# Kernel tuning notes

Hardware: AMD Instinct MI355X
Metric: run time of the kernel (lower is better)

Reference implementation:

```python
import math
import jax, jax.numpy as jnp
import numpy as np

B, T, D, S = 4, 8192, 1024, 32  # batch, seq, dim, num_slots; segment L = T // S


def setup_inputs() -> dict:
    key = jax.random.key(0)
    ks = jax.random.split(key, 11)
    d_inv_sqrt = D ** -0.5
    return {
        "x": jax.random.normal(ks[0], (B, T, D), jnp.float32),
        "gate_w": jax.random.normal(ks[1], (D, D), jnp.float32) * d_inv_sqrt,
        "gate_b": jnp.zeros((D,), jnp.float32),
        "read_q_w": jax.random.normal(ks[2], (D, D), jnp.float32) * 0.02,
        "read_k_w": jax.random.normal(ks[3], (D, D), jnp.float32) * 0.02,
        "read_v_w": jax.random.normal(ks[4], (D, D), jnp.float32) * 0.02,
        "output_w": jax.random.normal(ks[5], (D, D), jnp.float32) * d_inv_sqrt,
        "memory_slots": jax.random.normal(ks[6], (S, D), jnp.float32) * 0.02,
        "write_q_w": jax.random.normal(ks[7], (D, D), jnp.float32) * 0.02,
        "write_k_w": jax.random.normal(ks[8], (D, D), jnp.float32) * 0.02,
        "write_v_w": jax.random.normal(ks[9], (D, D), jnp.float32) * 0.02,
    }


def reference(x, gate_w, gate_b, read_q_w, read_k_w, read_v_w, output_w,
              memory_slots, write_q_w, write_k_w, write_v_w):
    b, t, d = x.shape
    s = memory_slots.shape[0]
    L = t // s  # segment length
    scale = 1.0 / math.sqrt(d)

    h = x @ gate_w.T + gate_b  # [B,T,D] gate pre-activation

    # --- write: per-slot attention over that slot's segment (block-diagonal) ---
    q = memory_slots @ write_q_w.T                      # [S,D]
    xs = x.reshape(b, s, L, d)                          # [B,S,L,D]
    k = xs @ write_k_w.T                                # [B,S,L,D]
    v = xs @ write_v_w.T                                # [B,S,L,D]
    wqk = jnp.einsum('sd,bsld->bsl', q, k) * scale      # [B,S,L]
    wattn = jax.nn.softmax(wqk, axis=-1)
    memory = jnp.einsum('bsl,bsld->bsd', wattn, v)      # [B,S,D]

    # --- read: masked cross-attention from tokens to memory slots ---
    rq = x @ read_q_w.T                                 # [B,T,D]
    rk = memory @ read_k_w.T                            # [B,S,D]
    rv = memory @ read_v_w.T                            # [B,S,D]
    rqk = jnp.einsum('btd,bsd->bts', rq, rk) * scale    # [B,T,S]
    seg = jnp.arange(t) // L                            # token -> segment index
    mask = seg[:, None] <= jnp.arange(s)[None, :]       # [T,S]; attend to slots >= own segment
    rqk = jnp.where(mask[None, :, :], rqk, -jnp.inf)
    rattn = jax.nn.softmax(rqk, axis=-1)
    read = jnp.einsum('bts,bsd->btd', rattn, rv)        # [B,T,D]

    y = x + jax.nn.sigmoid(h) * read
    out = y @ output_w.T
    return out, memory
```

## Files before the change

### kernel.cpp

```cpp
#include <hip/hip_runtime.h>
#include <stdint.h>

#define TB 4
#define TT 8192
#define TD 1024
#define TS 32
#define TL 256
#define BT 32768

typedef unsigned short u16;
typedef __bf16 bf16x8 __attribute__((ext_vector_type(8)));
typedef float f32x4 __attribute__((ext_vector_type(4)));

typedef uint32_t u32_g __attribute__((address_space(1)));
typedef uint32_t u32_l __attribute__((address_space(3)));

#define VMWAIT(N) asm volatile("s_waitcnt vmcnt(" #N ")" ::: "memory")
#define LGKM0()   asm volatile("s_waitcnt lgkmcnt(0)" ::: "memory")

__device__ __forceinline__ u16 f2b(float f){
  union { float f; uint32_t u; } a; a.f = f;
  uint32_t r = a.u + 0x7FFFu + ((a.u >> 16) & 1u);
  return (u16)(r >> 16);
}
__device__ __forceinline__ float b2f(u16 u){
  union { uint32_t u; float f; } a; a.u = ((uint32_t)u) << 16;
  return a.f;
}
__device__ __forceinline__ void gll16(const void* g, void* l){
  __builtin_amdgcn_global_load_lds((const u32_g*)g, (u32_l*)l, 16, 0, 0);
}
__device__ __forceinline__ bf16x8 cvt8(const float* p){
  float4 a = *(const float4*)p, b = *(const float4*)(p+4);
  union { u16 s[8]; bf16x8 v; } u;
  u.s[0]=f2b(a.x); u.s[1]=f2b(a.y); u.s[2]=f2b(a.z); u.s[3]=f2b(a.w);
  u.s[4]=f2b(b.x); u.s[5]=f2b(b.y); u.s[6]=f2b(b.z); u.s[7]=f2b(b.w);
  return u.v;
}

__global__ void k_convdot(const float* __restrict__ x, const float* __restrict__ qk,
                          u16* __restrict__ xb, float* __restrict__ wqk,
                          const float* __restrict__ s0, const float* __restrict__ s1,
                          const float* __restrict__ s2, const float* __restrict__ s3,
                          const float* __restrict__ s4,
                          u16* __restrict__ d0, u16* __restrict__ d1,
                          u16* __restrict__ d2, u16* __restrict__ d3,
                          u16* __restrict__ d4){
  int tid = threadIdx.x;
  if (blockIdx.x >= 2048){
    int i = (blockIdx.x - 2048)*256 + tid;
    int mi = i >> 18, j = i & 262143;
    const float* src; u16* dst;
    if      (mi == 0){ src = s0; dst = d0; }
    else if (mi == 1){ src = s1; dst = d1; }
    else if (mi == 2){ src = s2; dst = d2; }
    else if (mi == 3){ src = s3; dst = d3; }
    else             { src = s4; dst = d4; }
    float4 v = ((const float4*)src)[j];
    ushort4 u; u.x=f2b(v.x); u.y=f2b(v.y); u.z=f2b(v.z); u.w=f2b(v.w);
    ((ushort4*)dst)[j] = u;
    return;
  }
  int lane = tid & 63, wv = tid >> 6;
  long bt0 = (long)blockIdx.x * 16;
  int sseg = (int)((bt0 & (TT-1)) >> 8);
  float qv[16];
  #pragma unroll
  for (int i=0;i<4;i++){
    float4 t = *(const float4*)(qk + (size_t)sseg*TD + i*256 + lane*4);
    qv[i*4+0]=t.x; qv[i*4+1]=t.y; qv[i*4+2]=t.z; qv[i*4+3]=t.w;
  }
  for (int tok = wv; tok < 16; tok += 4){
    long bt = bt0 + tok;
    const float* xr = x + bt*TD;
    float dot = 0.f;
    #pragma unroll
    for (int i=0;i<4;i++){
      float4 t = *(const float4*)(xr + i*256 + lane*4);
      ushort4 u; u.x=f2b(t.x); u.y=f2b(t.y); u.z=f2b(t.z); u.w=f2b(t.w);
      *(ushort4*)(xb + bt*TD + i*256 + lane*4) = u;
      dot += t.x*qv[i*4] + t.y*qv[i*4+1] + t.z*qv[i*4+2] + t.w*qv[i*4+3];
    }
    #pragma unroll
    for (int o=32;o;o>>=1) dot += __shfl_xor(dot, o);
    if (lane == 0) wqk[bt] = dot;
  }
}

__global__ __launch_bounds__(512) void k_q32f(const float* __restrict__ ms, const float* __restrict__ Wq,
                                              float* __restrict__ q){
  int tid = threadIdx.x, lane = tid & 63, wv = tid >> 6;
  int r15 = lane & 15, kg = lane >> 4;
  int n0 = blockIdx.x*128 + wv*16;
  const float* ap = ms + (size_t)r15*TD + kg*8;
  const float* bp = Wq + (size_t)(n0 + r15)*TD + kg*8;
  f32x4 a0 = {0,0,0,0}, a1 = {0,0,0,0};
  #pragma unroll 4
  for (int k0=0; k0<TD; k0+=32){
    bf16x8 b  = cvt8(bp + k0);
    bf16x8 x0 = cvt8(ap + k0);
    bf16x8 x1 = cvt8(ap + 16*TD + k0);
    a0 = __builtin_amdgcn_mfma_f32_16x16x32_bf16(x0, b, a0, 0,0,0);
    a1 = __builtin_amdgcn_mfma_f32_16x16x32_bf16(x1, b, a1, 0,0,0);
  }
  #pragma unroll
  for (int qq=0; qq<4; ++qq){
    q[(size_t)(kg*4 + qq)*TD + n0 + r15]      = a0[qq];
    q[(size_t)(16 + kg*4 + qq)*TD + n0 + r15] = a1[qq];
  }
}

__global__ __launch_bounds__(512) void k_smm128(const u16* __restrict__ A,
                                                const u16* __restrict__ W0, const u16* __restrict__ W1,
                                                float* __restrict__ oF0, u16* __restrict__ oB0,
                                                u16* __restrict__ oBT1){
  int tid = threadIdx.x, lane = tid & 63, wv = tid >> 6;
  int r15 = lane & 15, kg = lane >> 4;
  int wr = wv >> 2, wc = wv & 3;
  int n0 = blockIdx.x*128 + wc*32;
  const u16* W = blockIdx.z ? W1 : W0;
  const u16* ap = A + (size_t)(wr*64 + r15)*TD + kg*8;
  const u16* bp = W + (size_t)(n0 + r15)*TD + kg*8;
  f32x4 acc[4][2];
  #pragma unroll
  for (int i=0;i<4;i++){ f32x4 z={0,0,0,0}; acc[i][0]=z; acc[i][1]=z; }
  #pragma unroll 2
  for (int k0=0; k0<TD; k0+=32){
    bf16x8 b0 = *(const bf16x8*)(bp + k0);
    bf16x8 b1 = *(const bf16x8*)(bp + 16*TD + k0);
    bf16x8 a0 = *(const bf16x8*)(ap + k0);
    bf16x8 a1 = *(const bf16x8*)(ap + 16*TD + k0);
    bf16x8 a2 = *(const bf16x8*)(ap + 32*TD + k0);
    bf16x8 a3 = *(const bf16x8*)(ap + 48*TD + k0);
    acc[0][0] = __builtin_amdgcn_mfma_f32_16x16x32_bf16(a0, b0, acc[0][0], 0,0,0);
    acc[0][1] = __builtin_amdgcn_mfma_f32_16x16x32_bf16(a0, b1, acc[0][1], 0,0,0);
    acc[1][0] = __builtin_amdgcn_mfma_f32_16x16x32_bf16(a1, b0, acc[1][0], 0,0,0);
    acc[1][1] = __builtin_amdgcn_mfma_f32_16x16x32_bf16(a1, b1, acc[1][1], 0,0,0);
    acc[2][0] = __builtin_amdgcn_mfma_f32_16x16x32_bf16(a2, b0, acc[2][0], 0,0,0);
    acc[2][1] = __builtin_amdgcn_mfma_f32_16x16x32_bf16(a2, b1, acc[2][1], 0,0,0);
    acc[3][0] = __builtin_amdgcn_mfma_f32_16x16x32_bf16(a3, b0, acc[3][0], 0,0,0);
    acc[3][1] = __builtin_amdgcn_mfma_f32_16x16x32_bf16(a3, b1, acc[3][1], 0,0,0);
  }
  #pragma unroll
  for (int mf=0; mf<4; ++mf){
    #pragma unroll
    for (int nf=0; nf<2; ++nf){
      int n = n0 + nf*16 + r15;
      #pragma unroll
      for (int qq=0; qq<4; ++qq){
        float v = acc[mf][nf][qq];
        int m = wr*64 + mf*16 + kg*4 + qq;
        if (blockIdx.z == 0){
          if (oF0) oF0[(size_t)m*TD + n] = v;
          if (oB0) oB0[(size_t)m*TD + n] = f2b(v);
        } else {
          oBT1[((size_t)(m>>5)*TD + n)*TS + (m&31)] = f2b(v);
        }
      }
    }
  }
}

__global__ void k_prep_qk(const float* __restrict__ q, const float* __restrict__ Wk,
                          float* __restrict__ qk){
  __shared__ float sq[TD];
  __shared__ f32x4 part[4][64];
  int s = blockIdx.x;
  int tid = threadIdx.x;
  int ds = tid >> 6, e4 = tid & 63;
  int e = blockIdx.y*256 + e4*4;
  for (int i = tid; i < TD; i += 256) sq[i] = q[s*TD + i];
  __syncthreads();
  f32x4 acc = {0,0,0,0};
  int d0 = ds*256;
  #pragma unroll 4
  for (int d = d0; d < d0+256; ++d){
    float4 w = *(const float4*)(Wk + (size_t)d*TD + e);
    float sv = sq[d];
    acc[0] += sv*w.x; acc[1] += sv*w.y; acc[2] += sv*w.z; acc[3] += sv*w.w;
  }
  part[ds][e4] = acc;
  __syncthreads();
  if (ds == 0){
    f32x4 t = part[0][e4];
    f32x4 t1 = part[1][e4], t2 = part[2][e4], t3 = part[3][e4];
    const float scale = 1.0f/32.0f;
    float4 o;
    o.x = (t[0]+t1[0]+t2[0]+t3[0])*scale;
    o.y = (t[1]+t1[1]+t2[1]+t3[1])*scale;
    o.z = (t[2]+t1[2]+t2[2]+t3[2])*scale;
    o.w = (t[3]+t1[3]+t2[3]+t3[3])*scale;
    *(float4*)(qk + (size_t)s*TD + e) = o;
  }
}

__global__ void k_wattn(const float* __restrict__ wqk, const u16* __restrict__ xb,
                        u16* __restrict__ xbarb){
  __shared__ float sw[TL];
  __shared__ float red[8];
  __shared__ f32x4 part[4][64];
  int tid = threadIdx.x, lane = tid & 63, wv = tid >> 6;
  int b = blockIdx.x >> 5, s = blockIdx.x & 31;
  long base = (long)b*TT + (long)s*TL;
  float v = wqk[base + tid];
  float m = v;
  #pragma unroll
  for (int o=32;o;o>>=1) m = fmaxf(m, __shfl_xor(m, o));
  if (lane == 0) red[wv] = m;
  __syncthreads();
  m = fmaxf(fmaxf(red[0], red[1]), fmaxf(red[2], red[3]));
  float e = __expf(v - m);
  float sm = e;
  #pragma unroll
  for (int o=32;o;o>>=1) sm += __shfl_xor(sm, o);
  if (lane == 0) red[4+wv] = sm;
  __syncthreads();
  sm = red[4]+red[5]+red[6]+red[7];
  sw[tid] = e / sm;
  __syncthreads();
  int d = blockIdx.y*256 + lane*4;
  const u16* xp = xb + (base + wv*64)*TD + d;
  f32x4 acc = {0,0,0,0};
  #pragma unroll 8
  for (int i=0; i<64; ++i){
    float w = sw[wv*64 + i];
    ushort4 u = *(const ushort4*)(xp + (size_t)i*TD);
    acc[0] += w*b2f(u.x); acc[1] += w*b2f(u.y); acc[2] += w*b2f(u.z); acc[3] += w*b2f(u.w);
  }
  part[wv][lane] = acc;
  __syncthreads();
  if (wv == 0){
    f32x4 t0 = part[0][lane], t1 = part[1][lane], t2 = part[2][lane], t3 = part[3][lane];
    ushort4 o;
    o.x = f2b(t0[0]+t1[0]+t2[0]+t3[0]);
    o.y = f2b(t0[1]+t1[1]+t2[1]+t3[1]);
    o.z = f2b(t0[2]+t1[2]+t2[2]+t3[2]);
    o.w = f2b(t0[3]+t1[3]+t2[3]+t3[3]);
    *(ushort4*)(xbarb + ((size_t)b*TS + s)*TD + d) = o;
  }
}

__global__ void k_mm(const float* __restrict__ A, const float* __restrict__ W,
                     int modeT, float scale,
                     float* __restrict__ Cf, float* __restrict__ Cf2,
                     u16* __restrict__ Cb, u16* __restrict__ CbT){
  __shared__ float sA[2][TD];
  int r0 = blockIdx.x*2;
  int n = blockIdx.y*256 + threadIdx.x;
  for (int i=threadIdx.x; i<2*TD; i+=256) sA[i>>10][i&1023] = A[(size_t)r0*TD + i];
  __syncthreads();
  float acc0=0.f, acc1=0.f;
  for (int k=0;k<TD;k+=4){
    float w0 = W[(size_t)k*TD + n],     w1 = W[(size_t)(k+1)*TD + n];
    float w2 = W[(size_t)(k+2)*TD + n], w3 = W[(size_t)(k+3)*TD + n];
    float4 a0 = *(const float4*)(&sA[0][k]);
    float4 a1 = *(const float4*)(&sA[1][k]);
    acc0 += w0*a0.x + w1*a0.y + w2*a0.z + w3*a0.w;
    acc1 += w0*a1.x + w1*a1.y + w2*a1.z + w3*a1.w;
  }
  #pragma unroll
  for (int r=0;r<2;r++){
    float v = (r==0?acc0:acc1)*scale;
    int rr = r0 + r;
    size_t idx = (size_t)rr*TD + n;
    if (Cf)  Cf[idx]  = v;
    if (Cb)  Cb[idx]  = f2b(v);
  }
}

__global__ __launch_bounds__(256) void k_pattn(const u16* __restrict__ xb, const u16* __restrict__ rkb,
                                               u16* __restrict__ P){
  int tid = threadIdx.x, lane = tid & 63, wv = tid >> 6;
  long bt0 = (long)blockIdx.x * 64;
  int b = (int)(bt0 >> 13);
  int smin = (int)((bt0 & (TT-1)) >> 8);
  int r15 = lane & 15, kg = lane >> 4;

  long tw = bt0 + wv*16;
  const u16* ap  = xb  + (size_t)(tw + r15)*TD + kg*8;
  const u16* bp0 = rkb + ((size_t)(b*TS + r15))*TD + kg*8;
  const u16* bp1 = rkb + ((size_t)(b*TS + 16 + r15))*TD + kg*8;
  f32x4 p0 = {0,0,0,0}, p1 = {0,0,0,0};
  #pragma unroll 4
  for (int ks=0; ks<32; ++ks){
    bf16x8 a  = *(const bf16x8*)(ap  + ks*32);
    bf16x8 b0 = *(const bf16x8*)(bp0 + ks*32);
    bf16x8 b1 = *(const bf16x8*)(bp1 + ks*32);
    p0 = __builtin_amdgcn_mfma_f32_16x16x32_bf16(a, b0, p0, 0,0,0);
    p1 = __builtin_amdgcn_mfma_f32_16x16x32_bf16(a, b1, p1, 0,0,0);
  }
  bool msk0 = (r15 < smin), msk1 = (16 + r15 < smin);
  #pragma unroll
  for (int q=0;q<4;q++){
    float l0 = msk0 ? -1e30f : p0[q];
    float l1 = msk1 ? -1e30f : p1[q];
    float mx = fmaxf(l0, l1);
    #pragma unroll
    for (int o=1;o<16;o<<=1) mx = fmaxf(mx, __shfl_xor(mx, o));
    float e0 = msk0 ? 0.f : __expf(l0 - mx);
    float e1 = msk1 ? 0.f : __expf(l1 - mx);
    float smv = e0 + e1;
    #pragma unroll
    for (int o=1;o<16;o<<=1) smv += __shfl_xor(smv, o);
    float rs = 1.f/smv;
    long trow = tw + 4*kg + q;
    P[trow*TS + r15]      = f2b(e0*rs);
    P[trow*TS + 16 + r15] = f2b(e1*rs);
  }
}

template<bool SIG>
__global__ __launch_bounds__(512, 2) void k_gemm(const u16* __restrict__ A, const u16* __restrict__ Bw,
                                                 const float* __restrict__ bias, void* __restrict__ Cp,
                                                 const u16* __restrict__ P, const u16* __restrict__ rvT){
  __shared__ __align__(16) char sL[131072];
  int tid = threadIdx.x, lane = tid & 63, wv = tid >> 6;
  int bid = blockIdx.x;
  int wg = ((bid & 7) << 6) | (bid >> 3);
  int nt = wg & 3, mt = wg >> 2;
  int m0 = mt*256, n0 = nt*256;
  int wr = wv >> 2, wc = wv & 3;
  int r15 = lane & 15, kg = lane >> 4;

  int ard[8], brd[4];
  #pragma unroll
  for (int i=0;i<8;i++){ int row = wr*128 + i*16 + r15; ard[i] = row*128 + ((kg ^ (row&7))<<4); }
  #pragma unroll
  for (int j=0;j<4;j++){ int row = wc*64  + j*16 + r15; brd[j] = row*128 + ((kg ^ (row&7))<<4); }

  const u16* asrc[4]; const u16* bsrc[4]; int ldst[4];
  #pragma unroll
  for (int r=0;r<4;r++){
    int Sp  = r*512 + tid;
    int row = Sp >> 3;
    int kq  = (Sp & 7) ^ (row & 7);
    asrc[r] = A  + (size_t)(m0 + row)*TD + kq*8;
    bsrc[r] = Bw + (size_t)(n0 + row)*TD + kq*8;
    ldst[r] = Sp*16;
  }

  f32x4 acc[8][4];
  #pragma unroll
  for (int i=0;i<8;i++){
    #pragma unroll
    for (int j=0;j<4;j++){ f32x4 z = {0,0,0,0}; acc[i][j] = z; }
  }

  auto stage = [&](int t){
    char* slot = sL + (size_t)(t&1)*65536;
    int k0 = t*64;
    #pragma unroll
    for (int r=0;r<4;r++) gll16(asrc[r] + k0, slot + ldst[r]);
    #pragma unroll
    for (int r=0;r<4;r++) gll16(bsrc[r] + k0, slot + 32768 + ldst[r]);
  };

  auto compute = [&](int t){
    const char* sa = sL + (size_t)(t&1)*65536;
    const char* sb = sa + 32768;
    bf16x8 bfg[4], af[4];
    #pragma unroll
    for (int j=0;j<4;j++) bfg[j] = *(const bf16x8*)(sb + brd[j]);
    #pragma unroll
    for (int i=0;i<4;i++) af[i] = *(const bf16x8*)(sa + ard[i]);
    LGKM0();
    __builtin_amdgcn_sched_barrier(0);
    __builtin_amdgcn_s_setprio(1);
    #pragma unroll
    for (int i=0;i<4;i++){
      #pragma unroll
      for (int j=0;j<4;j++)
        acc[i][j] = __builtin_amdgcn_mfma_f32_16x16x32_bf16(af[i], bfg[j], acc[i][j], 0,0,0);
    }
    __builtin_amdgcn_s_setprio(0);
    bf16x8 af2[4];
    #pragma unroll
    for (int i=0;i<4;i++) af2[i] = *(const bf16x8*)(sa + (ard[4+i]));
    LGKM0();
    __builtin_amdgcn_sched_barrier(0);
    __builtin_amdgcn_s_setprio(1);
    #pragma unroll
    for (int i=0;i<4;i++){
      #pragma unroll
      for (int j=0;j<4;j++)
        acc[4+i][j] = __builtin_amdgcn_mfma_f32_16x16x32_bf16(af2[i], bfg[j], acc[4+i][j], 0,0,0);
    }
    __builtin_amdgcn_s_setprio(0);
    bf16x8 bfh[4], ag[4];
    #pragma unroll
    for (int j=0;j<4;j++) bfh[j] = *(const bf16x8*)(sb + (brd[j]^64));
    #pragma unroll
    for (int i=0;i<4;i++) ag[i] = *(const bf16x8*)(sa + (ard[i]^64));
    LGKM0();
    __builtin_amdgcn_sched_barrier(0);
    __builtin_amdgcn_s_setprio(1);
    #pragma unroll
    for (int i=0;i<4;i++){
      #pragma unroll
      for (int j=0;j<4;j++)
        acc[i][j] = __builtin_amdgcn_mfma_f32_16x16x32_bf16(ag[i], bfh[j], acc[i][j], 0,0,0);
    }
    __builtin_amdgcn_s_setprio(0);
    bf16x8 ag2[4];
    #pragma unroll
    for (int i=0;i<4;i++) ag2[i] = *(const bf16x8*)(sa + (ard[4+i]^64));
    LGKM0();
    __builtin_amdgcn_sched_barrier(0);
    __builtin_amdgcn_s_setprio(1);
    #pragma unroll
    for (int i=0;i<4;i++){
      #pragma unroll
      for (int j=0;j<4;j++)
        acc[4+i][j] = __builtin_amdgcn_mfma_f32_16x16x32_bf16(ag2[i], bfh[j], acc[4+i][j], 0,0,0);
    }
    __builtin_amdgcn_s_setprio(0);
  };

  stage(0);
  for (int t=0; t<16; ++t){
    if (t > 0) __builtin_amdgcn_s_barrier();
    if (t < 15){
      stage(t+1);
      VMWAIT(8);
    } else {
      VMWAIT(0);
    }
    __builtin_amdgcn_s_barrier();
    compute(t);
  }

  if (SIG){
    int b = m0 >> 13;
    bf16x8 vfrag[4];
    #pragma unroll
    for (int j=0;j<4;j++){
      int n = n0 + wc*64 + j*16 + r15;
      vfrag[j] = *(const bf16x8*)(rvT + ((size_t)b*TD + n)*TS + kg*8);
    }
    #pragma unroll
    for (int i=0;i<8;i++){
      int tokbase = m0 + wr*128 + i*16;
      bf16x8 pfrag = *(const bf16x8*)(P + (size_t)(tokbase + r15)*TS + kg*8);
      f32x4 rd[4];
      #pragma unroll
      for (int j=0;j<4;j++){
        f32x4 z = {0,0,0,0};
        rd[j] = __builtin_amdgcn_mfma_f32_16x16x32_bf16(pfrag, vfrag[j], z, 0,0,0);
      }
      int mrow = tokbase + kg*4;
      #pragma unroll
      for (int j=0;j<4;j++){
        int n = n0 + wc*64 + j*16 + r15;
        float bj = bias[n];
        #pragma unroll
        for (int q=0;q<4;q++){
          float g = 1.f/(1.f + __expf(-(acc[i][j][q] + bj)));
          size_t idx = (size_t)(mrow + q)*TD + n;
          float xv = b2f(A[idx]);
          ((u16*)Cp)[idx] = f2b(xv + g*rd[j][q]);
        }
      }
    }
  } else {
    #pragma unroll
    for (int i=0;i<8;i++){
      int mrow = m0 + wr*128 + i*16 + kg*4;
      #pragma unroll
      for (int j=0;j<4;j++){
        int n = n0 + wc*64 + j*16 + r15;
        #pragma unroll
        for (int q=0;q<4;q++){
          size_t idx = (size_t)(mrow + q)*TD + n;
          ((float*)Cp)[idx] = acc[i][j][q];
        }
      }
    }
  }
}

extern "C" void kernel_launch(void* const* d_in, const int* in_sizes, int n_in,
                              void* d_out, int out_size, void* d_ws, size_t ws_size,
                              hipStream_t stream){
  const float* x   = (const float*)d_in[0];
  const float* gw  = (const float*)d_in[1];
  const float* gb  = (const float*)d_in[2];
  const float* rqw = (const float*)d_in[3];
  const float* rkw = (const float*)d_in[4];
  const float* rvw = (const float*)d_in[5];
  const float* ow  = (const float*)d_in[6];
  const float* ms  = (const float*)d_in[7];
  const float* wqw = (const float*)d_in[8];
  const float* wkw = (const float*)d_in[9];
  const float* wvw = (const float*)d_in[10];
  float* out = (float*)d_out;
  float* mem_out = out + (size_t)BT*TD;

  char* o = (char*)d_out;
  u16* xb    = (u16*)o;
  u16* Pb    = (u16*)(o + 67108864);
  u16* gwb   = (u16*)(o + 69206016);
  u16* wvwb  = (u16*)(o + 71303168);
  u16* rkwb  = (u16*)(o + 73400320);
  u16* rvwb  = (u16*)(o + 75497472);
  u16* xbarb = (u16*)(o + 79757312);
  u16* memb  = (u16*)(o + 80019456);
  u16* rvT   = (u16*)(o + 80281600);

  char* w = (char*)d_ws;
  u16*   gy    = (u16*)(w);
  float* wqkb  = (float*)(w + 67108864);
  float* qb    = (float*)(w + 67239936);
  float* qkb   = (float*)(w + 67371008);
  float* rkbf  = (float*)(w + 67502080);
  u16*   rkb   = (u16*)(w + 68026368);
  u16*   owb   = (u16*)(w + 68288512);

  k_q32f<<<8,512,0,stream>>>(ms, wqw, qb);
  k_prep_qk<<<dim3(32,4),256,0,stream>>>(qb, wkw, qkb);
  k_convdot<<<7168,256,0,stream>>>(x, qkb, xb, wqkb,
                                   gw, ow, wvw, rkw, rvw,
                                   gwb, owb, wvwb, rkwb, rvwb);
  k_wattn<<<dim3(128,4),256,0,stream>>>(wqkb, xb, xbarb);
  k_smm128<<<dim3(8,1,1),512,0,stream>>>(xbarb, wvwb, wvwb, mem_out, memb, nullptr);
  k_smm128<<<dim3(8,1,2),512,0,stream>>>(memb, rkwb, rvwb, rkbf, nullptr, rvT);
  k_mm<<<dim3(64,4),256,0,stream>>>(rkbf, rqw, 0, 1.f/32.f, nullptr, nullptr, rkb, nullptr);
  k_pattn<<<512,256,0,stream>>>(xb, rkb, Pb);
  k_gemm<true><<<512,512,0,stream>>>(xb, gwb, gb, gy, Pb, rvT);
  k_gemm<false><<<512,512,0,stream>>>(gy, owb, nullptr, d_out, nullptr, nullptr);
}
```

Baseline: 466.6 us.

## Precompose weight products so memory-side projections become one GEMM stage

Rewrites the small memory-side chain by composing weight matrices ahead of time: Wq·Wk is formed as one matrix, and Wk_read·Wv and Wv_read·Wv plus the read-query weight are composed into combined matrices. The read keys, read values and memory then all come from xbar in one batched launch. This replaces serial fp32 scalar kernels (k_prep_qk, k_mm) and a dependent GEMM chain with MFMA GEMMs on transposed bf16 weights. In exchange it adds several 1024x1024x1024 weight GEMMs plus transposes per call, and extra bf16 rounding of the composed weights, which may affect accuracy.

```diff
diff --git a/kernel.cpp b/kernel.cpp
--- a/kernel.cpp
+++ b/kernel.cpp
@@ -30,15 +30,122 @@
 __device__ __forceinline__ void gll16(const void* g, void* l){
   __builtin_amdgcn_global_load_lds((const u32_g*)g, (u32_l*)l, 16, 0, 0);
 }
-__device__ __forceinline__ bf16x8 cvt8(const float* p){
-  float4 a = *(const float4*)p, b = *(const float4*)(p+4);
-  union { u16 s[8]; bf16x8 v; } u;
-  u.s[0]=f2b(a.x); u.s[1]=f2b(a.y); u.s[2]=f2b(a.z); u.s[3]=f2b(a.w);
-  u.s[4]=f2b(b.x); u.s[5]=f2b(b.y); u.s[6]=f2b(b.z); u.s[7]=f2b(b.w);
-  return u.v;
-}
-
-__global__ void k_convdot(const float* __restrict__ x, const float* __restrict__ qk,
+
+__global__ void k_tran(const float* __restrict__ w0, const float* __restrict__ w1,
+                       const float* __restrict__ w2, const float* __restrict__ w3,
+                       const float* __restrict__ ms,
+                       u16* __restrict__ t0, u16* __restrict__ t1,
+                       u16* __restrict__ t2, u16* __restrict__ t3,
+                       u16* __restrict__ msb){
+  int tid = threadIdx.x, z = blockIdx.z;
+  if (z == 4){
+    int i = (blockIdx.y*16 + blockIdx.x)*256 + tid;
+    if (i < 8192){
+      float4 v = ((const float4*)ms)[i];
+      ushort4 u; u.x=f2b(v.x); u.y=f2b(v.y); u.z=f2b(v.z); u.w=f2b(v.w);
+      ((ushort4*)msb)[i] = u;
+    }
+    return;
+  }
+  const float* src = (z==0)?w0:(z==1)?w1:(z==2)?w2:w3;
+  u16* dst = (z==0)?t0:(z==1)?t1:(z==2)?t2:t3;
+  __shared__ float sT[64][65];
+  int r0 = blockIdx.y*64, c0 = blockIdx.x*64;
+  int lr = tid >> 2, lc = (tid & 3)*16;
+  #pragma unroll
+  for (int j=0; j<4; ++j){
+    float4 v = *(const float4*)(src + (size_t)(r0+lr)*TD + c0 + lc + j*4);
+    sT[lr][lc+j*4+0]=v.x; sT[lr][lc+j*4+1]=v.y; sT[lr][lc+j*4+2]=v.z; sT[lr][lc+j*4+3]=v.w;
+  }
+  __syncthreads();
+  int oc = tid >> 2, orh = (tid & 3)*16;
+  #pragma unroll
+  for (int j=0; j<4; ++j){
+    ushort4 u;
+    u.x = f2b(sT[orh+j*4+0][oc]);
+    u.y = f2b(sT[orh+j*4+1][oc]);
+    u.z = f2b(sT[orh+j*4+2][oc]);
+    u.w = f2b(sT[orh+j*4+3][oc]);
+    *(ushort4*)(dst + (size_t)(c0+oc)*TD + r0 + orh + j*4) = u;
+  }
+}
+
+__global__ __launch_bounds__(512) void k_smmw(
+    const u16* __restrict__ A0, const u16* __restrict__ W0, u16* __restrict__ O0, int tr0, float s0,
+    const u16* __restrict__ A1, const u16* __restrict__ W1, u16* __restrict__ O1, int tr1, float s1){
+  const u16 *A, *W; u16* O; int tr; float sc;
+  if (blockIdx.z == 0){ A=A0; W=W0; O=O0; tr=tr0; sc=s0; }
+  else                { A=A1; W=W1; O=O1; tr=tr1; sc=s1; }
+  int tid = threadIdx.x, lane = tid & 63, wv = tid >> 6;
+  int r15 = lane & 15, kg = lane >> 4;
+  int wr = wv >> 2, wc = wv & 3;
+  int m0 = blockIdx.y*128 + wr*64;
+  int n0 = blockIdx.x*128 + wc*32;
+  const u16* ap = A + (size_t)(m0 + r15)*TD + kg*8;
+  const u16* bp = W + (size_t)(n0 + r15)*TD + kg*8;
+  f32x4 acc[4][2];
+  #pragma unroll
+  for (int i=0;i<4;i++){ f32x4 z={0,0,0,0}; acc[i][0]=z; acc[i][1]=z; }
+  #pragma unroll 2
+  for (int k0=0; k0<TD; k0+=32){
+    bf16x8 b0 = *(const bf16x8*)(bp + k0);
+    bf16x8 b1 = *(const bf16x8*)(bp + 16*TD + k0);
+    bf16x8 a0 = *(const bf16x8*)(ap + k0);
+    bf16x8 a1 = *(const bf16x8*)(ap + 16*TD + k0);
+    bf16x8 a2 = *(const bf16x8*)(ap + 32*TD + k0);
+    bf16x8 a3 = *(const bf16x8*)(ap + 48*TD + k0);
+    acc[0][0] = __builtin_amdgcn_mfma_f32_16x16x32_bf16(a0, b0, acc[0][0], 0,0,0);
+    acc[0][1] = __builtin_amdgcn_mfma_f32_16x16x32_bf16(a0, b1, acc[0][1], 0,0,0);
+    acc[1][0] = __builtin_amdgcn_mfma_f32_16x16x32_bf16(a1, b0, acc[1][0], 0,0,0);
+    acc[1][1] = __builtin_amdgcn_mfma_f32_16x16x32_bf16(a1, b1, acc[1][1], 0,0,0);
+    acc[2][0] = __builtin_amdgcn_mfma_f32_16x16x32_bf16(a2, b0, acc[2][0], 0,0,0);
+    acc[2][1] = __builtin_amdgcn_mfma_f32_16x16x32_bf16(a2, b1, acc[2][1], 0,0,0);
+    acc[3][0] = __builtin_amdgcn_mfma_f32_16x16x32_bf16(a3, b0, acc[3][0], 0,0,0);
+    acc[3][1] = __builtin_amdgcn_mfma_f32_16x16x32_bf16(a3, b1, acc[3][1], 0,0,0);
+  }
+  #pragma unroll
+  for (int mf=0; mf<4; ++mf){
+    #pragma unroll
+    for (int nf=0; nf<2; ++nf){
+      int n = n0 + nf*16 + r15;
+      #pragma unroll
+      for (int qq=0; qq<4; ++qq){
+        float v = acc[mf][nf][qq]*sc;
+        int m = m0 + mf*16 + kg*4 + qq;
+        if (tr) O[(size_t)n*TD + m] = f2b(v);
+        else    O[(size_t)m*TD + n] = f2b(v);
+      }
+    }
+  }
+}
+
+__global__ __launch_bounds__(512) void k_qk32(const u16* __restrict__ msb, const u16* __restrict__ WzT,
+                                              float* __restrict__ qkp){
+  int tid = threadIdx.x, lane = tid & 63, wv = tid >> 6;
+  int r15 = lane & 15, kg = lane >> 4;
+  int n0 = blockIdx.x*128 + wv*16;
+  int kbase = blockIdx.y*512;
+  const u16* ap = msb + (size_t)r15*TD + kbase + kg*8;
+  const u16* bp = WzT + (size_t)(n0 + r15)*TD + kbase + kg*8;
+  f32x4 a0 = {0,0,0,0}, a1 = {0,0,0,0};
+  #pragma unroll 4
+  for (int k0=0; k0<512; k0+=32){
+    bf16x8 b  = *(const bf16x8*)(bp + k0);
+    bf16x8 x0 = *(const bf16x8*)(ap + k0);
+    bf16x8 x1 = *(const bf16x8*)(ap + 16*TD + k0);
+    a0 = __builtin_amdgcn_mfma_f32_16x16x32_bf16(x0, b, a0, 0,0,0);
+    a1 = __builtin_amdgcn_mfma_f32_16x16x32_bf16(x1, b, a1, 0,0,0);
+  }
+  const float sc = 1.0f/32.0f;
+  float* o = qkp + (size_t)blockIdx.y*32768;
+  #pragma unroll
+  for (int qq=0; qq<4; ++qq){
+    o[(size_t)(kg*4 + qq)*TD + n0 + r15]      = a0[qq]*sc;
+    o[(size_t)(16 + kg*4 + qq)*TD + n0 + r15] = a1[qq]*sc;
+  }
+}
+
+__global__ void k_convdot(const float* __restrict__ x, const float* __restrict__ qkp,
                           u16* __restrict__ xb, float* __restrict__ wqk,
                           const float* __restrict__ s0, const float* __restrict__ s1,
                           const float* __restrict__ s2, const float* __restrict__ s3,
@@ -67,8 +174,10 @@
   float qv[16];
   #pragma unroll
   for (int i=0;i<4;i++){
-    float4 t = *(const float4*)(qk + (size_t)sseg*TD + i*256 + lane*4);
-    qv[i*4+0]=t.x; qv[i*4+1]=t.y; qv[i*4+2]=t.z; qv[i*4+3]=t.w;
+    const float* qp = qkp + (size_t)sseg*TD + i*256 + lane*4;
+    float4 ta = *(const float4*)qp;
+    float4 tb = *(const float4*)(qp + 32768);
+    qv[i*4+0]=ta.x+tb.x; qv[i*4+1]=ta.y+tb.y; qv[i*4+2]=ta.z+tb.z; qv[i*4+3]=ta.w+tb.w;
   }
   for (int tok = wv; tok < 16; tok += 4){
     long bt = bt0 + tok;
@@ -87,43 +196,68 @@
   }
 }
 
-__global__ __launch_bounds__(512) void k_q32f(const float* __restrict__ ms, const float* __restrict__ Wq,
-                                              float* __restrict__ q){
+__global__ void k_wattn(const float* __restrict__ wqk, const u16* __restrict__ xb,
+                        u16* __restrict__ xbarb){
+  __shared__ float sw[TL];
+  __shared__ float red[8];
+  __shared__ f32x4 part[4][64];
   int tid = threadIdx.x, lane = tid & 63, wv = tid >> 6;
-  int r15 = lane & 15, kg = lane >> 4;
-  int n0 = blockIdx.x*128 + wv*16;
-  const float* ap = ms + (size_t)r15*TD + kg*8;
-  const float* bp = Wq + (size_t)(n0 + r15)*TD + kg*8;
-  f32x4 a0 = {0,0,0,0}, a1 = {0,0,0,0};
-  #pragma unroll 4
-  for (int k0=0; k0<TD; k0+=32){
-    bf16x8 b  = cvt8(bp + k0);
-    bf16x8 x0 = cvt8(ap + k0);
-    bf16x8 x1 = cvt8(ap + 16*TD + k0);
-    a0 = __builtin_amdgcn_mfma_f32_16x16x32_bf16(x0, b, a0, 0,0,0);
-    a1 = __builtin_amdgcn_mfma_f32_16x16x32_bf16(x1, b, a1, 0,0,0);
-  }
-  #pragma unroll
-  for (int qq=0; qq<4; ++qq){
-    q[(size_t)(kg*4 + qq)*TD + n0 + r15]      = a0[qq];
-    q[(size_t)(16 + kg*4 + qq)*TD + n0 + r15] = a1[qq];
-  }
-}
-
-__global__ __launch_bounds__(512) void k_smm128(const u16* __restrict__ A,
-                                                const u16* __restrict__ W0, const u16* __restrict__ W1,
-                                                float* __restrict__ oF0, u16* __restrict__ oB0,
-                                                u16* __restrict__ oBT1){
+  int b = blockIdx.x >> 5, s = blockIdx.x & 31;
+  long base = (long)b*TT + (long)s*TL;
+  float v = wqk[base + tid];
+  float m = v;
+  #pragma unroll
+  for (int o=32;o;o>>=1) m = fmaxf(m, __shfl_xor(m, o));
+  if (lane == 0) red[wv] = m;
+  __syncthreads();
+  m = fmaxf(fmaxf(red[0], red[1]), fmaxf(red[2], red[3]));
+  float e = __expf(v - m);
+  float sm = e;
+  #pragma unroll
+  for (int o=32;o;o>>=1) sm += __shfl_xor(sm, o);
+  if (lane == 0) red[4+wv] = sm;
+  __syncthreads();
+  sm = red[4]+red[5]+red[6]+red[7];
+  sw[tid] = e / sm;
+  __syncthreads();
+  int d = blockIdx.y*256 + lane*4;
+  const u16* xp = xb + (base + wv*64)*TD + d;
+  f32x4 acc = {0,0,0,0};
+  #pragma unroll 8
+  for (int i=0; i<64; ++i){
+    float w = sw[wv*64 + i];
+    ushort4 u = *(const ushort4*)(xp + (size_t)i*TD);
+    acc[0] += w*b2f(u.x); acc[1] += w*b2f(u.y); acc[2] += w*b2f(u.z); acc[3] += w*b2f(u.w);
+  }
+  part[wv][lane] = acc;
+  __syncthreads();
+  if (wv == 0){
+    f32x4 t0 = part[0][lane], t1 = part[1][lane], t2 = part[2][lane], t3 = part[3][lane];
+    ushort4 o;
+    o.x = f2b(t0[0]+t1[0]+t2[0]+t3[0]);
+    o.y = f2b(t0[1]+t1[1]+t2[1]+t3[1]);
+    o.z = f2b(t0[2]+t1[2]+t2[2]+t3[2]);
+    o.w = f2b(t0[3]+t1[3]+t2[3]+t3[3]);
+    *(ushort4*)(xbarb + ((size_t)b*TS + s)*TD + d) = o;
+  }
+}
+
+__global__ __launch_bounds__(512) void k_xbar3(const u16* __restrict__ xbarb,
+                                               const u16* __restrict__ Wv, const u16* __restrict__ WdT,
+                                               const u16* __restrict__ We,
+                                               float* __restrict__ memo, u16* __restrict__ rkb,
+                                               u16* __restrict__ rvT){
+  int z = blockIdx.z;
+  const u16* W = (z==0) ? Wv : (z==1) ? WdT : We;
   int tid = threadIdx.x, lane = tid & 63, wv = tid >> 6;
   int r15 = lane & 15, kg = lane >> 4;
   int wr = wv >> 2, wc = wv & 3;
   int n0 = blockIdx.x*128 + wc*32;
-  const u16* W = blockIdx.z ? W1 : W0;
-  const u16* ap = A + (size_t)(wr*64 + r15)*TD + kg*8;
+  const u16* ap = xbarb + (size_t)(wr*64 + r15)*TD + kg*8;
   const u16* bp = W + (size_t)(n0 + r15)*TD + kg*8;
   f32x4 acc[4][2];
   #pragma unroll
-  for (int i=0;i<4;i++){ f32x4 z={0,0,0,0}; acc[i][0]=z; acc[i][1]=z; }
+  for (int i=0;i<4;i++){ f32x4 zz={0,0,0,0}; acc[i][0]=zz; acc[i][1]=zz; }
   #pragma unroll 2
   for (int k0=0; k0<TD; k0+=32){
     bf16x8 b0 = *(const bf16x8*)(bp + k0);
@@ -150,121 +284,11 @@
       for (int qq=0; qq<4; ++qq){
         float v = acc[mf][nf][qq];
         int m = wr*64 + mf*16 + kg*4 + qq;
-        if (blockIdx.z == 0){
-          if (oF0) oF0[(size_t)m*TD + n] = v;
-          if (oB0) oB0[(size_t)m*TD + n] = f2b(v);
-        } else {
-          oBT1[((size_t)(m>>5)*TD + n)*TS + (m&31)] = f2b(v);
-        }
+        if (z == 0)      memo[(size_t)m*TD + n] = v;
+        else if (z == 1) rkb[(size_t)m*TD + n] = f2b(v);
+        else             rvT[((size_t)(m>>5)*TD + n)*TS + (m&31)] = f2b(v);
       }
     }
-  }
-}
-
-__global__ void k_prep_qk(const float* __restrict__ q, const float* __restrict__ Wk,
-                          float* __restrict__ qk){
-  __shared__ float sq[TD];
-  __shared__ f32x4 part[4][64];
-  int s = blockIdx.x;
-  int tid = threadIdx.x;
-  int ds = tid >> 6, e4 = tid & 63;
-  int e = blockIdx.y*256 + e4*4;
-  for (int i = tid; i < TD; i += 256) sq[i] = q[s*TD + i];
-  __syncthreads();
-  f32x4 acc = {0,0,0,0};
-  int d0 = ds*256;
-  #pragma unroll 4
-  for (int d = d0; d < d0+256; ++d){
-    float4 w = *(const float4*)(Wk + (size_t)d*TD + e);
-    float sv = sq[d];
-    acc[0] += sv*w.x; acc[1] += sv*w.y; acc[2] += sv*w.z; acc[3] += sv*w.w;
-  }
-  part[ds][e4] = acc;
-  __syncthreads();
-  if (ds == 0){
-    f32x4 t = part[0][e4];
-    f32x4 t1 = part[1][e4], t2 = part[2][e4], t3 = part[3][e4];
-    const float scale = 1.0f/32.0f;
-    float4 o;
-    o.x = (t[0]+t1[0]+t2[0]+t3[0])*scale;
-    o.y = (t[1]+t1[1]+t2[1]+t3[1])*scale;
-    o.z = (t[2]+t1[2]+t2[2]+t3[2])*scale;
-    o.w = (t[3]+t1[3]+t2[3]+t3[3])*scale;
-    *(float4*)(qk + (size_t)s*TD + e) = o;
-  }
-}
-
-__global__ void k_wattn(const float* __restrict__ wqk, const u16* __restrict__ xb,
-                        u16* __restrict__ xbarb){
-  __shared__ float sw[TL];
-  __shared__ float red[8];
-  __shared__ f32x4 part[4][64];
-  int tid = threadIdx.x, lane = tid & 63, wv = tid >> 6;
-  int b = blockIdx.x >> 5, s = blockIdx.x & 31;
-  long base = (long)b*TT + (long)s*TL;
-  float v = wqk[base + tid];
-  float m = v;
-  #pragma unroll
-  for (int o=32;o;o>>=1) m = fmaxf(m, __shfl_xor(m, o));
-  if (lane == 0) red[wv] = m;
-  __syncthreads();
-  m = fmaxf(fmaxf(red[0], red[1]), fmaxf(red[2], red[3]));
-  float e = __expf(v - m);
-  float sm = e;
-  #pragma unroll
-  for (int o=32;o;o>>=1) sm += __shfl_xor(sm, o);
-  if (lane == 0) red[4+wv] = sm;
-  __syncthreads();
-  sm = red[4]+red[5]+red[6]+red[7];
-  sw[tid] = e / sm;
-  __syncthreads();
-  int d = blockIdx.y*256 + lane*4;
-  const u16* xp = xb + (base + wv*64)*TD + d;
-  f32x4 acc = {0,0,0,0};
-  #pragma unroll 8
-  for (int i=0; i<64; ++i){
-    float w = sw[wv*64 + i];
-    ushort4 u = *(const ushort4*)(xp + (size_t)i*TD);
-    acc[0] += w*b2f(u.x); acc[1] += w*b2f(u.y); acc[2] += w*b2f(u.z); acc[3] += w*b2f(u.w);
-  }
-  part[wv][lane] = acc;
-  __syncthreads();
-  if (wv == 0){
-    f32x4 t0 = part[0][lane], t1 = part[1][lane], t2 = part[2][lane], t3 = part[3][lane];
-    ushort4 o;
-    o.x = f2b(t0[0]+t1[0]+t2[0]+t3[0]);
-    o.y = f2b(t0[1]+t1[1]+t2[1]+t3[1]);
-    o.z = f2b(t0[2]+t1[2]+t2[2]+t3[2]);
-    o.w = f2b(t0[3]+t1[3]+t2[3]+t3[3]);
-    *(ushort4*)(xbarb + ((size_t)b*TS + s)*TD + d) = o;
-  }
-}
-
-__global__ void k_mm(const float* __restrict__ A, const float* __restrict__ W,
-                     int modeT, float scale,
-                     float* __restrict__ Cf, float* __restrict__ Cf2,
-                     u16* __restrict__ Cb, u16* __restrict__ CbT){
-  __shared__ float sA[2][TD];
-  int r0 = blockIdx.x*2;
-  int n = blockIdx.y*256 + threadIdx.x;
-  for (int i=threadIdx.x; i<2*TD; i+=256) sA[i>>10][i&1023] = A[(size_t)r0*TD + i];
-  __syncthreads();
-  float acc0=0.f, acc1=0.f;
-  for (int k=0;k<TD;k+=4){
-    float w0 = W[(size_t)k*TD + n],     w1 = W[(size_t)(k+1)*TD + n];
-    float w2 = W[(size_t)(k+2)*TD + n], w3 = W[(size_t)(k+3)*TD + n];
-    float4 a0 = *(const float4*)(&sA[0][k]);
-    float4 a1 = *(const float4*)(&sA[1][k]);
-    acc0 += w0*a0.x + w1*a0.y + w2*a0.z + w3*a0.w;
-    acc1 += w0*a1.x + w1*a1.y + w2*a1.z + w3*a1.w;
-  }
-  #pragma unroll
-  for (int r=0;r<2;r++){
-    float v = (r==0?acc0:acc1)*scale;
-    int rr = r0 + r;
-    size_t idx = (size_t)rr*TD + n;
-    if (Cf)  Cf[idx]  = v;
-    if (Cb)  Cb[idx]  = f2b(v);
   }
 }
 
@@ -503,27 +527,34 @@
   u16* rkwb  = (u16*)(o + 73400320);
   u16* rvwb  = (u16*)(o + 75497472);
   u16* xbarb = (u16*)(o + 79757312);
-  u16* memb  = (u16*)(o + 80019456);
   u16* rvT   = (u16*)(o + 80281600);
+  u16* WvT   = (u16*)(o + 84934656);
+  u16* WrqT  = (u16*)(o + 87031808);
+  u16* WqT   = (u16*)(o + 89128960);
+  u16* WkT   = (u16*)(o + 91226112);
+  u16* WhT   = (u16*)(o + 93323264);
+  u16* We    = (u16*)(o + 95420416);
+  u16* WdT   = (u16*)(o + 97517568);
+  u16* WzT   = (u16*)(o + 99614720);
+  u16* msb   = (u16*)(o + 101711872);
 
   char* w = (char*)d_ws;
   u16*   gy    = (u16*)(w);
   float* wqkb  = (float*)(w + 67108864);
-  float* qb    = (float*)(w + 67239936);
-  float* qkb   = (float*)(w + 67371008);
-  float* rkbf  = (float*)(w + 67502080);
-  u16*   rkb   = (u16*)(w + 68026368);
+  float* qkp   = (float*)(w + 67239936);
+  u16*   rkb   = (u16*)(w + 67502080);
   u16*   owb   = (u16*)(w + 68288512);
 
-  k_q32f<<<8,512,0,stream>>>(ms, wqw, qb);
-  k_prep_qk<<<dim3(32,4),256,0,stream>>>(qb, wkw, qkb);
-  k_convdot<<<7168,256,0,stream>>>(x, qkb, xb, wqkb,
+  k_tran<<<dim3(16,16,5),256,0,stream>>>(wvw, rqw, wqw, wkw, ms, WvT, WrqT, WqT, WkT, msb);
+  k_smmw<<<dim3(8,8,1),512,0,stream>>>(WqT, WkT, WzT, 1, 1.f,  WqT, WkT, WzT, 1, 1.f);
+  k_qk32<<<dim3(8,2),512,0,stream>>>(msb, WzT, qkp);
+  k_convdot<<<7168,256,0,stream>>>(x, qkp, xb, wqkb,
                                    gw, ow, wvw, rkw, rvw,
                                    gwb, owb, wvwb, rkwb, rvwb);
   k_wattn<<<dim3(128,4),256,0,stream>>>(wqkb, xb, xbarb);
-  k_smm128<<<dim3(8,1,1),512,0,stream>>>(xbarb, wvwb, wvwb, mem_out, memb, nullptr);
-  k_smm128<<<dim3(8,1,2),512,0,stream>>>(memb, rkwb, rvwb, rkbf, nullptr, rvT);
-  k_mm<<<dim3(64,4),256,0,stream>>>(rkbf, rqw, 0, 1.f/32.f, nullptr, nullptr, rkb, nullptr);
+  k_smmw<<<dim3(8,8,2),512,0,stream>>>(rkwb, WvT, WhT, 1, 1.f,  rvwb, WvT, We, 0, 1.f);
+  k_smmw<<<dim3(8,8,1),512,0,stream>>>(WhT, WrqT, WdT, 1, 1.f/32.f,  WhT, WrqT, WdT, 1, 1.f/32.f);
+  k_xbar3<<<dim3(8,1,3),512,0,stream>>>(xbarb, wvwb, WdT, We, mem_out, rkb, rvT);
   k_pattn<<<512,256,0,stream>>>(xb, rkb, Pb);
   k_gemm<true><<<512,512,0,stream>>>(xb, gwb, gb, gy, Pb, rvT);
   k_gemm<false><<<512,512,0,stream>>>(gy, owb, nullptr, d_out, nullptr, nullptr);
```

Result: faster. 451.4 us (-3.2%).
